# Performance work log

Hardware: AMD Instinct MI355X
Metric: run time of the kernel (lower is better)

## Reference

```python
import jax, jax.numpy as jnp
import numpy as np

B, T, D = 8, 1024, 1024
H, G = 16, 4            # num_heads, query_groups
HD = D // H             # head_dim = 64
REP = H // G            # heads_per_group
EPS = 1e-10
NEG = -1e9


def setup_inputs() -> dict:
    key = jax.random.key(0)
    k1, k2, k3 = jax.random.split(key, 3)
    x = jax.random.normal(k1, (B, T, D), dtype=jnp.float32)
    w_qkv = jax.random.normal(k2, (D, H * HD + 2 * G * HD), dtype=jnp.float32) * (D ** -0.5)
    w_o = jax.random.normal(k3, (D, D), dtype=jnp.float32) * (D ** -0.5)
    padding_mask = jnp.ones((B, T), dtype=bool)
    return {"x": x, "w_qkv": w_qkv, "w_o": w_o, "padding_mask": padding_mask}


def _l2_norm(t):
    # qk_norm_type=2: L2 normalize over head_dim
    return t / (jnp.sqrt(jnp.sum(t * t, axis=-1, keepdims=True)) + EPS)


def reference(x, w_qkv, w_o, padding_mask):
    # fused QKV projection: [B,T,D] @ [D, H*HD + 2*G*HD]
    qkv = x @ w_qkv
    q, k, v = jnp.split(qkv, [H * HD, H * HD + G * HD], axis=-1)
    q = q.reshape(B, T, H, HD)
    k = k.reshape(B, T, G, HD)
    v = v.reshape(B, T, G, HD)
    # QK normalization (L2 over head_dim)
    q = _l2_norm(q)
    k = _l2_norm(k)
    # GQA: expand KV heads (repeat_interleave along head dim)
    k = jnp.repeat(k, REP, axis=2)  # [B,T,H,HD]
    v = jnp.repeat(v, REP, axis=2)
    # to [B,H,T,HD]
    q = q.transpose(0, 2, 1, 3)
    k = k.transpose(0, 2, 1, 3)
    v = v.transpose(0, 2, 1, 3)
    # causal + padding mask, True = attend
    causal = jnp.tril(jnp.ones((T, T), dtype=bool))  # [T_q, T_k]
    valid = padding_mask[:, None, :, None] & padding_mask[:, None, None, :] & causal[None, None]
    scale = HD ** -0.5  # SDPA default scale
    scores = jnp.einsum('bhqd,bhkd->bhqk', q, k) * scale
    scores = jnp.where(valid, scores, NEG)
    attn = jax.nn.softmax(scores, axis=-1)
    out = jnp.einsum('bhqk,bhkd->bhqd', attn, v)  # [B,H,T,HD]
    out = out.transpose(0, 2, 1, 3).reshape(B, T, D)
    return out @ w_o
```

## Files before the change

### kernel.cpp

```cpp
#include <hip/hip_runtime.h>
#include <hip/hip_bf16.h>

typedef __attribute__((ext_vector_type(8))) short short8;
typedef __attribute__((ext_vector_type(4))) float f32x4;

#define B_ 8
#define T_ 1024
#define D_ 1024
#define H_ 16
#define G_ 4
#define HD_ 64
#define QKVW 1536

#define GLOAD16(gp, lp) __builtin_amdgcn_global_load_lds( \
    (const __attribute__((address_space(1))) void*)(gp),  \
    (__attribute__((address_space(3))) void*)(lp), 16, 0, 0)

__device__ __forceinline__ float exp2_fast(float x) {
    return __builtin_amdgcn_exp2f(x);
}

__global__ __launch_bounds__(256) void cvt_f32_bf16(
    const float* __restrict__ in, __hip_bfloat16* __restrict__ out, int n)
{
    int i = (blockIdx.x * 256 + threadIdx.x) * 8;
    if (i >= n) return;
    float4 a = *reinterpret_cast<const float4*>(in + i);
    float4 b = *reinterpret_cast<const float4*>(in + i + 4);
    union { short8 s; __hip_bfloat16 h[8]; } u;
    u.h[0] = __float2bfloat16(a.x); u.h[1] = __float2bfloat16(a.y);
    u.h[2] = __float2bfloat16(a.z); u.h[3] = __float2bfloat16(a.w);
    u.h[4] = __float2bfloat16(b.x); u.h[5] = __float2bfloat16(b.y);
    u.h[6] = __float2bfloat16(b.z); u.h[7] = __float2bfloat16(b.w);
    *reinterpret_cast<short8*>(out + i) = u.s;
}

__global__ __launch_bounds__(256) void cvt_transpose(
    const float* __restrict__ in, __hip_bfloat16* __restrict__ outT, int K, int N)
{
    __shared__ float tile[32][33];
    const int k0 = blockIdx.y * 32, n0 = blockIdx.x * 32;
    const int r = threadIdx.x >> 5, c = threadIdx.x & 31;
    #pragma unroll
    for (int i = 0; i < 4; ++i)
        tile[r + i * 8][c] = in[(size_t)(k0 + r + i * 8) * N + n0 + c];
    __syncthreads();
    #pragma unroll
    for (int i = 0; i < 4; ++i)
        outT[(size_t)(n0 + r + i * 8) * K + k0 + c] = __float2bfloat16(tile[c][r + i * 8]);
}

template <typename CT>
__global__ __launch_bounds__(256) void gemm_tn(
    const __hip_bfloat16* __restrict__ A,
    const __hip_bfloat16* __restrict__ Bt,
    CT* __restrict__ C, int M, int N, int K)
{
    __shared__ __hip_bfloat16 As[2][128 * 32];
    __shared__ __hip_bfloat16 Bs[2][128 * 32];

    const int tid  = threadIdx.x;
    const int lane = tid & 63;
    const int wr   = (tid >> 6) >> 1;
    const int wc   = (tid >> 6) & 1;

    const int NBY = M >> 7;
    const int rpx = NBY >> 3;
    const int xcd = blockIdx.x & 7;
    const int lin = blockIdx.x >> 3;
    const int by  = xcd * rpx + (lin % rpx);
    const int bx  = lin / rpx;
    const int m0 = by * 128;
    const int n0 = bx * 128;

    f32x4 acc[4][4] = {};

    const int s0 = tid * 8,          sr0 = s0 >> 5, sc0 = s0 & 31;
    const int s1 = (256 + tid) * 8,  sr1 = s1 >> 5, sc1 = s1 & 31;

    const __hip_bfloat16* Ar0 = A  + (size_t)(m0 + sr0) * K + sc0;
    const __hip_bfloat16* Ar1 = A  + (size_t)(m0 + sr1) * K + sc1;
    const __hip_bfloat16* Br0 = Bt + (size_t)(n0 + sr0) * K + sc0;
    const __hip_bfloat16* Br1 = Bt + (size_t)(n0 + sr1) * K + sc1;

    const int fr = lane & 15;
    const int kf = (lane >> 4) * 8;

    GLOAD16(Ar0, &As[0][s0]);
    GLOAD16(Ar1, &As[0][s1]);
    GLOAD16(Br0, &Bs[0][s0]);
    GLOAD16(Br1, &Bs[0][s1]);
    __syncthreads();

    int cur = 0;
    for (int kk = 0; kk < K; kk += 32) {
        const int nxt = cur ^ 1;
        if (kk + 32 < K) {
            GLOAD16(Ar0 + kk + 32, &As[nxt][s0]);
            GLOAD16(Ar1 + kk + 32, &As[nxt][s1]);
            GLOAD16(Br0 + kk + 32, &Bs[nxt][s0]);
            GLOAD16(Br1 + kk + 32, &Bs[nxt][s1]);
        }
        short8 a[4], b[4];
        #pragma unroll
        for (int m = 0; m < 4; ++m)
            a[m] = *reinterpret_cast<const short8*>(&As[cur][(wr * 64 + m * 16 + fr) * 32 + kf]);
        #pragma unroll
        for (int n = 0; n < 4; ++n)
            b[n] = *reinterpret_cast<const short8*>(&Bs[cur][(wc * 64 + n * 16 + fr) * 32 + kf]);
        #pragma unroll
        for (int m = 0; m < 4; ++m)
            #pragma unroll
            for (int n = 0; n < 4; ++n)
                acc[m][n] = __builtin_amdgcn_mfma_f32_16x16x32_bf16(a[m], b[n], acc[m][n], 0, 0, 0);
        __syncthreads();
        cur = nxt;
    }

    const int rowb = m0 + wr * 64 + (lane >> 4) * 4;
    const int colb = n0 + wc * 64 + fr;
    #pragma unroll
    for (int m = 0; m < 4; ++m)
        #pragma unroll
        for (int n = 0; n < 4; ++n)
            #pragma unroll
            for (int r = 0; r < 4; ++r) {
                float v = acc[m][n][r];
                if constexpr (__is_same(CT, float))
                    C[(size_t)(rowb + m * 16 + r) * N + colb + n * 16] = v;
                else
                    C[(size_t)(rowb + m * 16 + r) * N + colb + n * 16] = __float2bfloat16(v);
            }
}

__global__ __launch_bounds__(256) void l2norm_qk(__hip_bfloat16* __restrict__ qkv)
{
    const int tid = threadIdx.x;
    const int vec = blockIdx.x * 32 + (tid >> 3);
    const int j   = tid & 7;
    const int NQ  = B_ * T_ * H_;

    size_t base;
    float extra;
    if (vec < NQ) {
        int bt = vec >> 4, h = vec & 15;
        base = (size_t)bt * QKVW + h * HD_;
        extra = 0.125f * 1.44269504f;
    } else {
        int v = vec - NQ;
        int bt = v >> 2, g = v & 3;
        base = (size_t)bt * QKVW + H_ * HD_ + g * HD_;
        extra = 1.0f;
    }

    union { short8 s; __hip_bfloat16 h[8]; } u;
    u.s = *reinterpret_cast<const short8*>(qkv + base + j * 8);
    float f[8], ss = 0.f;
    #pragma unroll
    for (int i = 0; i < 8; ++i) { f[i] = __bfloat162float(u.h[i]); ss += f[i] * f[i]; }
    ss += __shfl_xor(ss, 1, 64);
    ss += __shfl_xor(ss, 2, 64);
    ss += __shfl_xor(ss, 4, 64);
    float sc = extra / (sqrtf(ss) + 1e-10f);
    #pragma unroll
    for (int i = 0; i < 8; ++i) u.h[i] = __float2bfloat16(f[i] * sc);
    *reinterpret_cast<short8*>(qkv + base + j * 8) = u.s;
}

__global__ __launch_bounds__(256) void vt_build(
    const __hip_bfloat16* __restrict__ qkv, __hip_bfloat16* __restrict__ vt)
{
    __shared__ __hip_bfloat16 tile[32][33];
    const int t0 = blockIdx.x * 32;
    const int d0 = blockIdx.y * 32;
    const int bg = blockIdx.z;
    const int r = threadIdx.x >> 5, c = threadIdx.x & 31;
    #pragma unroll
    for (int i = 0; i < 4; ++i)
        tile[r + i * 8][c] = qkv[((size_t)((bg >> 2) * T_ + t0 + r + i * 8)) * QKVW
                                 + (H_ + G_) * HD_ + (bg & 3) * HD_ + d0 + c];
    __syncthreads();
    #pragma unroll
    for (int i = 0; i < 4; ++i)
        vt[((size_t)(bg * HD_ + d0 + r + i * 8)) * T_ + t0 + c] = tile[c][r + i * 8];
}

__global__ __launch_bounds__(256) void attn_fwd(
    const __hip_bfloat16* __restrict__ qkv,
    const __hip_bfloat16* __restrict__ vt,
    __hip_bfloat16* __restrict__ out)
{
    const int pair = blockIdx.x;
    const int h  = blockIdx.y;
    const int b  = blockIdx.z;
    const int g  = h >> 2;

    const int tid  = threadIdx.x;
    const int lane = tid & 63;
    const int wid  = tid >> 6;

    __shared__ __hip_bfloat16 Ks[64][88];
    __shared__ __hip_bfloat16 Vs[64][88];
    __shared__ __hip_bfloat16 Ps[4][16][88];

    const int kf = (lane >> 4) * 8;
    const int fr = lane & 15;

    const int s0 = tid * 8,          sr0 = s0 >> 6, sc0 = s0 & 63;
    const int s1 = (256 + tid) * 8,  sr1 = s1 >> 6, sc1 = s1 & 63;

    const size_t krow0 = (size_t)(b * T_ + sr0) * QKVW + H_ * HD_ + g * HD_ + sc0;
    const size_t krow1 = (size_t)(b * T_ + sr1) * QKVW + H_ * HD_ + g * HD_ + sc1;
    const size_t vrow0 = (size_t)((b * G_ + g) * HD_ + sr0) * T_ + sc0;
    const size_t vrow1 = (size_t)((b * G_ + g) * HD_ + sr1) * T_ + sc1;

    for (int half = 0; half < 2; ++half) {
        const int qt = half ? (15 - pair) : pair;
        const int q0 = qt * 64;
        const int arow  = q0 + wid * 16 + fr;
        const int rbase = q0 + wid * 16 + (lane >> 4) * 4;

        short8 qfrag0, qfrag1;
        {
            const size_t qbase = ((size_t)(b * T_ + arow)) * QKVW + h * HD_;
            qfrag0 = *reinterpret_cast<const short8*>(qkv + qbase + kf);
            qfrag1 = *reinterpret_cast<const short8*>(qkv + qbase + 32 + kf);
        }

        float lsum[4] = {0.f, 0.f, 0.f, 0.f};
        f32x4 o[4] = {};

        {
            short8 k0 = *reinterpret_cast<const short8*>(qkv + krow0);
            short8 k1 = *reinterpret_cast<const short8*>(qkv + krow1);
            short8 v0 = *reinterpret_cast<const short8*>(vt + vrow0);
            short8 v1 = *reinterpret_cast<const short8*>(vt + vrow1);
            *reinterpret_cast<short8*>(&Ks[sr0][sc0]) = k0;
            *reinterpret_cast<short8*>(&Ks[sr1][sc1]) = k1;
            *reinterpret_cast<short8*>(&Vs[sr0][sc0]) = v0;
            *reinterpret_cast<short8*>(&Vs[sr1][sc1]) = v1;
        }
        __syncthreads();

        for (int kt = 0; kt <= qt; ++kt) {
            const bool diag = (kt == qt);
            const bool more = (kt < qt);

            short8 nk0, nk1, nv0, nv1;
            if (more) {
                const size_t koff = (size_t)((kt + 1) * 64) * QKVW;
                nk0 = *reinterpret_cast<const short8*>(qkv + krow0 + koff);
                nk1 = *reinterpret_cast<const short8*>(qkv + krow1 + koff);
                nv0 = *reinterpret_cast<const short8*>(vt + vrow0 + (kt + 1) * 64);
                nv1 = *reinterpret_cast<const short8*>(vt + vrow1 + (kt + 1) * 64);
            }

            f32x4 s[4] = {};
            #pragma unroll
            for (int nf = 0; nf < 4; ++nf) {
                short8 b0 = *reinterpret_cast<const short8*>(&Ks[fr + 16 * nf][kf]);
                short8 b1 = *reinterpret_cast<const short8*>(&Ks[fr + 16 * nf][32 + kf]);
                s[nf] = __builtin_amdgcn_mfma_f32_16x16x32_bf16(qfrag0, b0, s[nf], 0, 0, 0);
                s[nf] = __builtin_amdgcn_mfma_f32_16x16x32_bf16(qfrag1, b1, s[nf], 0, 0, 0);
            }

            if (diag) {
                #pragma unroll
                for (int nf = 0; nf < 4; ++nf) {
                    int col = kt * 64 + fr + 16 * nf;
                    #pragma unroll
                    for (int r = 0; r < 4; ++r) {
                        float p = (col <= rbase + r) ? exp2_fast(s[nf][r]) : 0.f;
                        lsum[r] += p;
                        Ps[wid][(lane >> 4) * 4 + r][fr + 16 * nf] = __float2bfloat16(p);
                    }
                }
            } else {
                #pragma unroll
                for (int nf = 0; nf < 4; ++nf)
                    #pragma unroll
                    for (int r = 0; r < 4; ++r) {
                        float p = exp2_fast(s[nf][r]);
                        lsum[r] += p;
                        Ps[wid][(lane >> 4) * 4 + r][fr + 16 * nf] = __float2bfloat16(p);
                    }
            }

            short8 pa0 = *reinterpret_cast<const short8*>(&Ps[wid][fr][kf]);
            short8 pa1 = *reinterpret_cast<const short8*>(&Ps[wid][fr][32 + kf]);
            #pragma unroll
            for (int nf = 0; nf < 4; ++nf) {
                short8 b0 = *reinterpret_cast<const short8*>(&Vs[fr + 16 * nf][kf]);
                short8 b1 = *reinterpret_cast<const short8*>(&Vs[fr + 16 * nf][32 + kf]);
                o[nf] = __builtin_amdgcn_mfma_f32_16x16x32_bf16(pa0, b0, o[nf], 0, 0, 0);
                o[nf] = __builtin_amdgcn_mfma_f32_16x16x32_bf16(pa1, b1, o[nf], 0, 0, 0);
            }
            __syncthreads();

            if (more) {
                *reinterpret_cast<short8*>(&Ks[sr0][sc0]) = nk0;
                *reinterpret_cast<short8*>(&Ks[sr1][sc1]) = nk1;
                *reinterpret_cast<short8*>(&Vs[sr0][sc0]) = nv0;
                *reinterpret_cast<short8*>(&Vs[sr1][sc1]) = nv1;
                __syncthreads();
            }
        }

        float linv[4];
        #pragma unroll
        for (int r = 0; r < 4; ++r) {
            float v = lsum[r];
            v += __shfl_xor(v, 1, 64);
            v += __shfl_xor(v, 2, 64);
            v += __shfl_xor(v, 4, 64);
            v += __shfl_xor(v, 8, 64);
            linv[r] = 1.0f / v;
        }
        #pragma unroll
        for (int nf = 0; nf < 4; ++nf) {
            int col = fr + 16 * nf;
            #pragma unroll
            for (int r = 0; r < 4; ++r) {
                float v = o[nf][r] * linv[r];
                out[((size_t)(b * T_ + rbase + r)) * (H_ * HD_) + h * HD_ + col] =
                    __float2bfloat16(v);
            }
        }
    }
}

extern "C" void kernel_launch(void* const* d_in, const int* in_sizes, int n_in,
                              void* d_out, int out_size, void* d_ws, size_t ws_size,
                              hipStream_t stream) {
    const float* x_f     = (const float*)d_in[0];
    const float* w_qkv_f = (const float*)d_in[1];
    const float* w_o_f   = (const float*)d_in[2];
    float* out = (float*)d_out;

    const int NX  = B_ * T_ * D_;
    const int NWQ = D_ * QKVW;
    const int NWO = D_ * D_;

    __hip_bfloat16* xb    = (__hip_bfloat16*)d_ws;
    __hip_bfloat16* wqkvT = xb + NX;
    __hip_bfloat16* woT   = wqkvT + NWQ;
    __hip_bfloat16* qkv   = woT + NWO;
    __hip_bfloat16* vt    = qkv + (size_t)(B_ * T_) * QKVW;
    __hip_bfloat16* attn_out = xb;

    dim3 blk(256);

    cvt_f32_bf16<<<dim3(NX / 2048), blk, 0, stream>>>(x_f, xb, NX);
    cvt_transpose<<<dim3(QKVW / 32, D_ / 32), blk, 0, stream>>>(w_qkv_f, wqkvT, D_, QKVW);
    cvt_transpose<<<dim3(D_ / 32, D_ / 32), blk, 0, stream>>>(w_o_f, woT, D_, D_);

    gemm_tn<__hip_bfloat16><<<dim3((QKVW / 128) * ((B_ * T_) / 128)), blk, 0, stream>>>(
        xb, wqkvT, qkv, B_ * T_, QKVW, D_);

    l2norm_qk<<<dim3((B_ * T_ * H_ + B_ * T_ * G_) / 32), blk, 0, stream>>>(qkv);

    vt_build<<<dim3(T_ / 32, HD_ / 32, B_ * G_), blk, 0, stream>>>(qkv, vt);

    attn_fwd<<<dim3(8, H_, B_), blk, 0, stream>>>(qkv, vt, attn_out);

    gemm_tn<float><<<dim3((D_ / 128) * ((B_ * T_) / 128)), blk, 0, stream>>>(
        attn_out, woT, out, B_ * T_, D_, D_);
}
```

Before: 136.6 us.

## Load K/V tiles via global_load_lds with XOR-swizzled unpadded LDS layout

```diff
diff --git a/kernel.cpp b/kernel.cpp
--- a/kernel.cpp
+++ b/kernel.cpp
@@ -199,20 +199,24 @@
     const int lane = tid & 63;
     const int wid  = tid >> 6;
 
-    __shared__ __hip_bfloat16 Ks[64][88];
-    __shared__ __hip_bfloat16 Vs[64][88];
-    __shared__ __hip_bfloat16 Ps[4][16][88];
-
-    const int kf = (lane >> 4) * 8;
-    const int fr = lane & 15;
-
-    const int s0 = tid * 8,          sr0 = s0 >> 6, sc0 = s0 & 63;
-    const int s1 = (256 + tid) * 8,  sr1 = s1 >> 6, sc1 = s1 & 63;
-
-    const size_t krow0 = (size_t)(b * T_ + sr0) * QKVW + H_ * HD_ + g * HD_ + sc0;
-    const size_t krow1 = (size_t)(b * T_ + sr1) * QKVW + H_ * HD_ + g * HD_ + sc1;
-    const size_t vrow0 = (size_t)((b * G_ + g) * HD_ + sr0) * T_ + sc0;
-    const size_t vrow1 = (size_t)((b * G_ + g) * HD_ + sr1) * T_ + sc1;
+    __shared__ __hip_bfloat16 Ks[64 * 64];
+    __shared__ __hip_bfloat16 Vs[64 * 64];
+    __shared__ __hip_bfloat16 Ps[4 * 16 * 64];
+
+    const int fr  = lane & 15;
+    const int kf  = (lane >> 4) * 8;
+    const int kb  = kf * 2;
+    const int swz = (fr & 7) << 4;
+
+    const int srow = tid >> 3;
+    const int scol = ((tid & 7) * 8) ^ ((srow & 7) << 3);
+
+    const size_t kgbase = (size_t)(b * T_) * QKVW + H_ * HD_ + g * HD_ + scol;
+    const size_t vgbase = (size_t)((b * G_ + g) * HD_) * T_ + scol;
+
+    char* KsB = (char*)Ks;
+    char* VsB = (char*)Vs;
+    char* PsB = (char*)Ps + wid * 2048;
 
     for (int half = 0; half < 2; ++half) {
         const int qt = half ? (15 - pair) : pair;
@@ -230,36 +234,21 @@
         float lsum[4] = {0.f, 0.f, 0.f, 0.f};
         f32x4 o[4] = {};
 
-        {
-            short8 k0 = *reinterpret_cast<const short8*>(qkv + krow0);
-            short8 k1 = *reinterpret_cast<const short8*>(qkv + krow1);
-            short8 v0 = *reinterpret_cast<const short8*>(vt + vrow0);
-            short8 v1 = *reinterpret_cast<const short8*>(vt + vrow1);
-            *reinterpret_cast<short8*>(&Ks[sr0][sc0]) = k0;
-            *reinterpret_cast<short8*>(&Ks[sr1][sc1]) = k1;
-            *reinterpret_cast<short8*>(&Vs[sr0][sc0]) = v0;
-            *reinterpret_cast<short8*>(&Vs[sr1][sc1]) = v1;
-        }
-        __syncthreads();
-
         for (int kt = 0; kt <= qt; ++kt) {
             const bool diag = (kt == qt);
-            const bool more = (kt < qt);
-
-            short8 nk0, nk1, nv0, nv1;
-            if (more) {
-                const size_t koff = (size_t)((kt + 1) * 64) * QKVW;
-                nk0 = *reinterpret_cast<const short8*>(qkv + krow0 + koff);
-                nk1 = *reinterpret_cast<const short8*>(qkv + krow1 + koff);
-                nv0 = *reinterpret_cast<const short8*>(vt + vrow0 + (kt + 1) * 64);
-                nv1 = *reinterpret_cast<const short8*>(vt + vrow1 + (kt + 1) * 64);
-            }
+
+            GLOAD16(qkv + kgbase + (size_t)(kt * 64 + srow) * QKVW,      &Ks[tid * 8]);
+            GLOAD16(qkv + kgbase + (size_t)(kt * 64 + 32 + srow) * QKVW, &Ks[2048 + tid * 8]);
+            GLOAD16(vt + vgbase + (size_t)srow * T_ + kt * 64,           &Vs[tid * 8]);
+            GLOAD16(vt + vgbase + (size_t)(32 + srow) * T_ + kt * 64,    &Vs[2048 + tid * 8]);
+            __syncthreads();
 
             f32x4 s[4] = {};
             #pragma unroll
             for (int nf = 0; nf < 4; ++nf) {
-                short8 b0 = *reinterpret_cast<const short8*>(&Ks[fr + 16 * nf][kf]);
-                short8 b1 = *reinterpret_cast<const short8*>(&Ks[fr + 16 * nf][32 + kf]);
+                const int row = fr + 16 * nf;
+                short8 b0 = *reinterpret_cast<const short8*>(KsB + row * 128 + (kb ^ swz));
+                short8 b1 = *reinterpret_cast<const short8*>(KsB + row * 128 + ((64 + kb) ^ swz));
                 s[nf] = __builtin_amdgcn_mfma_f32_16x16x32_bf16(qfrag0, b0, s[nf], 0, 0, 0);
                 s[nf] = __builtin_amdgcn_mfma_f32_16x16x32_bf16(qfrag1, b1, s[nf], 0, 0, 0);
             }
@@ -272,7 +261,9 @@
                     for (int r = 0; r < 4; ++r) {
                         float p = (col <= rbase + r) ? exp2_fast(s[nf][r]) : 0.f;
                         lsum[r] += p;
-                        Ps[wid][(lane >> 4) * 4 + r][fr + 16 * nf] = __float2bfloat16(p);
+                        int q = (lane >> 4) * 4 + r;
+                        *(__hip_bfloat16*)(PsB + q * 128 +
+                            ((2 * (fr + 16 * nf)) ^ ((q & 7) << 4))) = __float2bfloat16(p);
                     }
                 }
             } else {
@@ -282,28 +273,23 @@
                     for (int r = 0; r < 4; ++r) {
                         float p = exp2_fast(s[nf][r]);
                         lsum[r] += p;
-                        Ps[wid][(lane >> 4) * 4 + r][fr + 16 * nf] = __float2bfloat16(p);
+                        int q = (lane >> 4) * 4 + r;
+                        *(__hip_bfloat16*)(PsB + q * 128 +
+                            ((2 * (fr + 16 * nf)) ^ ((q & 7) << 4))) = __float2bfloat16(p);
                     }
             }
 
-            short8 pa0 = *reinterpret_cast<const short8*>(&Ps[wid][fr][kf]);
-            short8 pa1 = *reinterpret_cast<const short8*>(&Ps[wid][fr][32 + kf]);
+            short8 pa0 = *reinterpret_cast<const short8*>(PsB + fr * 128 + (kb ^ swz));
+            short8 pa1 = *reinterpret_cast<const short8*>(PsB + fr * 128 + ((64 + kb) ^ swz));
             #pragma unroll
             for (int nf = 0; nf < 4; ++nf) {
-                short8 b0 = *reinterpret_cast<const short8*>(&Vs[fr + 16 * nf][kf]);
-                short8 b1 = *reinterpret_cast<const short8*>(&Vs[fr + 16 * nf][32 + kf]);
+                const int row = fr + 16 * nf;
+                short8 b0 = *reinterpret_cast<const short8*>(VsB + row * 128 + (kb ^ swz));
+                short8 b1 = *reinterpret_cast<const short8*>(VsB + row * 128 + ((64 + kb) ^ swz));
                 o[nf] = __builtin_amdgcn_mfma_f32_16x16x32_bf16(pa0, b0, o[nf], 0, 0, 0);
                 o[nf] = __builtin_amdgcn_mfma_f32_16x16x32_bf16(pa1, b1, o[nf], 0, 0, 0);
             }
             __syncthreads();
-
-            if (more) {
-                *reinterpret_cast<short8*>(&Ks[sr0][sc0]) = nk0;
-                *reinterpret_cast<short8*>(&Ks[sr1][sc1]) = nk1;
-                *reinterpret_cast<short8*>(&Vs[sr0][sc0]) = nv0;
-                *reinterpret_cast<short8*>(&Vs[sr1][sc1]) = nv1;
-                __syncthreads();
-            }
         }
 
         float linv[4];
```

Result: no change. 134.0 us (-1.9%).
